# Performance work log

Measured on AMD Instinct MI355X. Metric: run time of the kernel, lower is better.

## Reference

```python
import jax, jax.numpy as jnp
import numpy as np

N_NODES, N_EDGES, D, N_RELS = 50000, 600000, 128, 460


def setup_inputs() -> dict:
    key = jax.random.key(0)
    ks = jax.random.split(key, 8)
    h = jax.random.normal(ks[0], (N_NODES, D), dtype=jnp.float32)
    emb_rel = jax.random.normal(ks[1], (N_RELS, D), dtype=jnp.float32)
    attn_fc_w = jax.random.normal(ks[2], (D, 3 * D), dtype=jnp.float32) * 0.05   # Linear(3D->D), weight [out,in]
    attn_fc2_w = jax.random.normal(ks[3], (1, D), dtype=jnp.float32) * 0.05     # Linear(D->1)
    loop_weight = jax.random.normal(ks[4], (D, D), dtype=jnp.float32) * 0.05
    edge_src = jax.random.randint(ks[5], (N_EDGES,), 0, N_NODES)
    edge_dst = jax.random.randint(ks[6], (N_EDGES,), 0, N_NODES)
    edge_type = jax.random.randint(ks[7], (N_EDGES,), 0, N_RELS)
    return {"h": h, "emb_rel": emb_rel, "attn_fc_w": attn_fc_w,
            "attn_fc2_w": attn_fc2_w, "loop_weight": loop_weight,
            "edge_src": edge_src, "edge_dst": edge_dst, "edge_type": edge_type}


def reference(h, emb_rel, attn_fc_w, attn_fc2_w, loop_weight, edge_src, edge_dst, edge_type):
    n = h.shape[0]
    # --- per-edge gather ---
    hs = h[edge_src]            # [E, D] src features (mailbox 'e_h')
    ht = h[edge_dst]            # [E, D]
    rel = emb_rel[edge_type]    # [E, D]
    # --- concat-MLP attention: leaky_relu(fc2(fc1([hs|ht|rel]))) ---
    z2 = jnp.concatenate([hs, ht, rel], axis=1)          # [E, 3D]
    a = z2 @ attn_fc_w.T                                  # [E, D]
    e = jax.nn.leaky_relu(a @ attn_fc2_w.T)               # [E, 1], slope 0.01 (torch default)
    # --- per-destination segment softmax ---
    m = jax.ops.segment_max(e, edge_dst, num_segments=n)  # [N, 1]
    m = jnp.where(jnp.isfinite(m), m, jnp.float32(0.0))   # empty nodes -> -inf; neutralize
    ex = jnp.exp(e - m[edge_dst])                         # [E, 1]
    den = jax.ops.segment_sum(ex, edge_dst, num_segments=n)
    alpha = ex / den[edge_dst]                            # [E, 1]
    # --- weighted scatter-sum of src features ---
    node_repr = jax.ops.segment_sum(alpha * hs, edge_dst, num_segments=n)  # [N, D]
    # --- self-loop ---
    node_repr = node_repr + h @ loop_weight
    return node_repr
```

## Files before the change

kernel.cpp:

```cpp
#include <hip/hip_runtime.h>

#define N_NODES 50000
#define N_EDGES 600000
#define D 128
#define N_RELS 460
#define CAP_LOG 6

typedef unsigned short u16;
typedef __attribute__((ext_vector_type(8))) short bf16x8;
typedef __attribute__((ext_vector_type(4))) float f32x4;

enum : int {
    OFF_W      = 0,
    OFF_S1     = 384,
    OFF_S2     = 50384,
    OFF_S3     = 100384,
    OFF_COUNTS = 100864,
    OFF_CSR    = 900864,
    OFF_HB     = 4100864,
    OFF_WT     = 7300864,
};

#define NODE_WAVES   12500
#define REL_WAVES    115
#define SCORE_BLOCKS 3154
#define ZERO_BLOCKS  3125
#define FILL_BLOCKS  1172
#define GEMM_BLOCKS  782

__device__ __forceinline__ u16 f2bf(float f) {
    unsigned u = __float_as_uint(f);
    unsigned r = u + 0x7FFFu + ((u >> 16) & 1u);
    return (u16)(r >> 16);
}

__global__ void k_prep(const float* __restrict__ fc1, const float* __restrict__ fc2,
                       const float* __restrict__ W,
                       float* __restrict__ w, u16* __restrict__ wt,
                       int* __restrict__ counts) {
    int b = blockIdx.x, t = threadIdx.x;
    if (b == 0) {
        for (int j = t; j < 3 * D; j += 256) {
            float acc = 0.f;
            for (int k = 0; k < D; ++k) acc += fc2[k] * fc1[k * 3 * D + j];
            w[j] = acc;
        }
    } else if (b <= 64) {
        int i = (b - 1) * 256 + t;
        int k = i >> 7, n = i & 127;
        wt[n * D + k] = f2bf(W[k * D + n]);
    } else {
        int i = (b - 65) * 256 + t;
        if (i < N_NODES * 16) counts[i] = 0;
    }
}

__global__ __launch_bounds__(256) void k_fused(
        const int* __restrict__ src, const int* __restrict__ dst,
        const int* __restrict__ typ, int* __restrict__ counts,
        unsigned* __restrict__ csr,
        const float* __restrict__ h, const float* __restrict__ emb_rel,
        const float* __restrict__ w,
        float* __restrict__ s1, float* __restrict__ s2, float* __restrict__ s3,
        u16* __restrict__ hb, const u16* __restrict__ wt,
        float* __restrict__ out) {
    if (blockIdx.x < FILL_BLOCKS) {
        int i = blockIdx.x * blockDim.x + threadIdx.x;
        if (i >= N_EDGES / 2) return;
        int2 d2  = ((const int2*)dst)[i];
        int2 s2v = ((const int2*)src)[i];
        int2 t2  = ((const int2*)typ)[i];
        int slot0 = atomicAdd(&counts[d2.x << 4], 1);
        int slot1 = atomicAdd(&counts[d2.y << 4], 1);
        csr[(d2.x << CAP_LOG) + slot0] = (unsigned)s2v.x | ((unsigned)t2.x << 16);
        csr[(d2.y << CAP_LOG) + slot1] = (unsigned)s2v.y | ((unsigned)t2.y << 16);
    } else if (blockIdx.x < FILL_BLOCKS + GEMM_BLOCKS) {
        int b = blockIdx.x - FILL_BLOCKS;
        int t = threadIdx.x;
        int wave = t >> 6, lane = t & 63;
        int quad = lane >> 4, m16 = lane & 15;
        int nbase = b * 64 + wave * 16;

        f32x4 acc[8];
        #pragma unroll
        for (int cg = 0; cg < 8; ++cg) acc[cg] = (f32x4){0.f, 0.f, 0.f, 0.f};

        int arow = nbase + m16;
        if (arow >= N_NODES) arow = N_NODES - 1;
        const float* aptr = h + (size_t)arow * D + quad * 8;

        #pragma unroll
        for (int k0 = 0; k0 < D; k0 += 32) {
            float4 a0 = *(const float4*)(aptr + k0);
            float4 a1 = *(const float4*)(aptr + k0 + 4);
            bf16x8 a;
            a[0] = (short)f2bf(a0.x); a[1] = (short)f2bf(a0.y);
            a[2] = (short)f2bf(a0.z); a[3] = (short)f2bf(a0.w);
            a[4] = (short)f2bf(a1.x); a[5] = (short)f2bf(a1.y);
            a[6] = (short)f2bf(a1.z); a[7] = (short)f2bf(a1.w);
            #pragma unroll
            for (int cg = 0; cg < 8; ++cg) {
                bf16x8 bb = *(const bf16x8*)(&wt[(size_t)(cg * 16 + m16) * D + k0 + quad * 8]);
                acc[cg] = __builtin_amdgcn_mfma_f32_16x16x32_bf16(a, bb, acc[cg], 0, 0, 0);
            }
        }
        #pragma unroll
        for (int reg = 0; reg < 4; ++reg) {
            int row = nbase + quad * 4 + reg;
            if (row < N_NODES) {
                #pragma unroll
                for (int cg = 0; cg < 8; ++cg)
                    out[(size_t)row * D + cg * 16 + m16] = acc[cg][reg];
            }
        }
    } else {
        int wv = ((blockIdx.x - FILL_BLOCKS - GEMM_BLOCKS) * blockDim.x + threadIdx.x) >> 6;
        int l  = threadIdx.x & 63;
        int sub = l >> 4;
        int q   = l & 15;
        if (wv < NODE_WAVES) {
            int r = wv * 4 + sub;
            const float* hp = h + (size_t)r * D + q * 8;
            float4 h0 = *(const float4*)hp;
            float4 h1 = *(const float4*)(hp + 4);
            uint4 pk;
            pk.x = (unsigned)f2bf(h0.x) | ((unsigned)f2bf(h0.y) << 16);
            pk.y = (unsigned)f2bf(h0.z) | ((unsigned)f2bf(h0.w) << 16);
            pk.z = (unsigned)f2bf(h1.x) | ((unsigned)f2bf(h1.y) << 16);
            pk.w = (unsigned)f2bf(h1.z) | ((unsigned)f2bf(h1.w) << 16);
            ((uint4*)hb)[(size_t)r * 16 + q] = pk;
            float4 w10 = *(const float4*)(w + q * 8);
            float4 w11 = *(const float4*)(w + q * 8 + 4);
            float4 w20 = *(const float4*)(w + D + q * 8);
            float4 w21 = *(const float4*)(w + D + q * 8 + 4);
            float a1 = h0.x * w10.x + h0.y * w10.y + h0.z * w10.z + h0.w * w10.w
                     + h1.x * w11.x + h1.y * w11.y + h1.z * w11.z + h1.w * w11.w;
            float a2 = h0.x * w20.x + h0.y * w20.y + h0.z * w20.z + h0.w * w20.w
                     + h1.x * w21.x + h1.y * w21.y + h1.z * w21.z + h1.w * w21.w;
            #pragma unroll
            for (int o = 8; o; o >>= 1) { a1 += __shfl_xor(a1, o, 16); a2 += __shfl_xor(a2, o, 16); }
            if (q == 0) { s1[r] = a1; s2[r] = a2; }
        } else if (wv < NODE_WAVES + REL_WAVES) {
            int r = (wv - NODE_WAVES) * 4 + sub;
            const float* rp = emb_rel + (size_t)r * D + q * 8;
            float4 r0 = *(const float4*)rp;
            float4 r1 = *(const float4*)(rp + 4);
            float4 w30 = *(const float4*)(w + 2 * D + q * 8);
            float4 w31 = *(const float4*)(w + 2 * D + q * 8 + 4);
            float a3 = r0.x * w30.x + r0.y * w30.y + r0.z * w30.z + r0.w * w30.w
                     + r1.x * w31.x + r1.y * w31.y + r1.z * w31.z + r1.w * w31.w;
            #pragma unroll
            for (int o = 8; o; o >>= 1) a3 += __shfl_xor(a3, o, 16);
            if (q == 0) s3[r] = a3;
        }
    }
}

__global__ void k_gather(const u16* __restrict__ hb, const int* __restrict__ counts,
                         const unsigned* __restrict__ csr,
                         const float* __restrict__ s1, const float* __restrict__ s2,
                         const float* __restrict__ s3, float* __restrict__ out) {
    int n  = (blockIdx.x * blockDim.x + threadIdx.x) >> 4;
    int gl = threadIdx.x & 15;
    if (n >= N_NODES) return;
    int deg = counts[n << 4];
    if (deg == 0) return;
    int beg = n << CAP_LOG;
    int end = beg + deg;

    float s2n = s2[n];
    float den = 0.f;
    f32x4 accA = {0.f, 0.f, 0.f, 0.f}, accB = {0.f, 0.f, 0.f, 0.f};

    for (int cb = beg; cb < end; cb += 16) {
        int i = cb + gl;
        int msrc = 0; float mex = 0.f;
        if (i < end) {
            unsigned p = csr[i];
            msrc = (int)(p & 0xFFFFu);
            float x = s1[msrc] + s2n + s3[p >> 16];
            float lv = (x > 0.f) ? x : 0.01f * x;
            mex = __expf(lv);
        }
        den += mex;
        int cnt = min(16, end - cb);
        int j = 0;
        for (; j + 3 < cnt; j += 4) {
            int   a0 = __shfl(msrc, j, 16),     a1 = __shfl(msrc, j + 1, 16);
            int   a2 = __shfl(msrc, j + 2, 16), a3 = __shfl(msrc, j + 3, 16);
            float c0 = __shfl(mex, j, 16),      c1 = __shfl(mex, j + 1, 16);
            float c2 = __shfl(mex, j + 2, 16),  c3 = __shfl(mex, j + 3, 16);
            uint4 u0 = ((const uint4*)(hb + (size_t)a0 * D))[gl];
            uint4 u1 = ((const uint4*)(hb + (size_t)a1 * D))[gl];
            uint4 u2 = ((const uint4*)(hb + (size_t)a2 * D))[gl];
            uint4 u3 = ((const uint4*)(hb + (size_t)a3 * D))[gl];
            accA.x += c0 * __uint_as_float(u0.x << 16) + c1 * __uint_as_float(u1.x << 16)
                    + c2 * __uint_as_float(u2.x << 16) + c3 * __uint_as_float(u3.x << 16);
            accA.y += c0 * __uint_as_float(u0.x & 0xFFFF0000u) + c1 * __uint_as_float(u1.x & 0xFFFF0000u)
                    + c2 * __uint_as_float(u2.x & 0xFFFF0000u) + c3 * __uint_as_float(u3.x & 0xFFFF0000u);
            accA.z += c0 * __uint_as_float(u0.y << 16) + c1 * __uint_as_float(u1.y << 16)
                    + c2 * __uint_as_float(u2.y << 16) + c3 * __uint_as_float(u3.y << 16);
            accA.w += c0 * __uint_as_float(u0.y & 0xFFFF0000u) + c1 * __uint_as_float(u1.y & 0xFFFF0000u)
                    + c2 * __uint_as_float(u2.y & 0xFFFF0000u) + c3 * __uint_as_float(u3.y & 0xFFFF0000u);
            accB.x += c0 * __uint_as_float(u0.z << 16) + c1 * __uint_as_float(u1.z << 16)
                    + c2 * __uint_as_float(u2.z << 16) + c3 * __uint_as_float(u3.z << 16);
            accB.y += c0 * __uint_as_float(u0.z & 0xFFFF0000u) + c1 * __uint_as_float(u1.z & 0xFFFF0000u)
                    + c2 * __uint_as_float(u2.z & 0xFFFF0000u) + c3 * __uint_as_float(u3.z & 0xFFFF0000u);
            accB.z += c0 * __uint_as_float(u0.w << 16) + c1 * __uint_as_float(u1.w << 16)
                    + c2 * __uint_as_float(u2.w << 16) + c3 * __uint_as_float(u3.w << 16);
            accB.w += c0 * __uint_as_float(u0.w & 0xFFFF0000u) + c1 * __uint_as_float(u1.w & 0xFFFF0000u)
                    + c2 * __uint_as_float(u2.w & 0xFFFF0000u) + c3 * __uint_as_float(u3.w & 0xFFFF0000u);
        }
        for (; j < cnt; ++j) {
            int   a0 = __shfl(msrc, j, 16);
            float c0 = __shfl(mex, j, 16);
            uint4 u0 = ((const uint4*)(hb + (size_t)a0 * D))[gl];
            accA.x += c0 * __uint_as_float(u0.x << 16);
            accA.y += c0 * __uint_as_float(u0.x & 0xFFFF0000u);
            accA.z += c0 * __uint_as_float(u0.y << 16);
            accA.w += c0 * __uint_as_float(u0.y & 0xFFFF0000u);
            accB.x += c0 * __uint_as_float(u0.z << 16);
            accB.y += c0 * __uint_as_float(u0.z & 0xFFFF0000u);
            accB.z += c0 * __uint_as_float(u0.w << 16);
            accB.w += c0 * __uint_as_float(u0.w & 0xFFFF0000u);
        }
    }
    #pragma unroll
    for (int o = 8; o; o >>= 1) den += __shfl_xor(den, o, 16);
    float inv = 1.f / den;

    float* op = out + (size_t)n * D + gl * 8;
    float4 o0 = *(float4*)op, o1 = *(float4*)(op + 4);
    o0.x += accA.x * inv; o0.y += accA.y * inv; o0.z += accA.z * inv; o0.w += accA.w * inv;
    o1.x += accB.x * inv; o1.y += accB.y * inv; o1.z += accB.z * inv; o1.w += accB.w * inv;
    *(float4*)op = o0; *(float4*)(op + 4) = o1;
}

extern "C" void kernel_launch(void* const* d_in, const int* in_sizes, int n_in,
                              void* d_out, int out_size, void* d_ws, size_t ws_size,
                              hipStream_t stream) {
    const float* h       = (const float*)d_in[0];
    const float* emb_rel = (const float*)d_in[1];
    const float* fc1     = (const float*)d_in[2];
    const float* fc2     = (const float*)d_in[3];
    const float* loopw   = (const float*)d_in[4];
    const int*   esrc    = (const int*)d_in[5];
    const int*   edst    = (const int*)d_in[6];
    const int*   etyp    = (const int*)d_in[7];
    float* out = (float*)d_out;
    float* ws  = (float*)d_ws;

    float*    w       = ws + OFF_W;
    float*    s1      = ws + OFF_S1;
    float*    s2      = ws + OFF_S2;
    float*    s3      = ws + OFF_S3;
    int*      counts  = (int*)(ws + OFF_COUNTS);
    unsigned* csr     = (unsigned*)(ws + OFF_CSR);
    u16*      hb      = (u16*)(ws + OFF_HB);
    u16*      wt      = (u16*)(ws + OFF_WT);

    k_prep<<<1 + 64 + ZERO_BLOCKS, 256, 0, stream>>>(fc1, fc2, loopw, w, wt, counts);

    k_fused<<<FILL_BLOCKS + GEMM_BLOCKS + SCORE_BLOCKS, 256, 0, stream>>>(
        esrc, edst, etyp, counts, csr, h, emb_rel, w, s1, s2, s3, hb, wt, out);

    k_gather<<<(N_NODES * 16 + 255) / 256, 256, 0, stream>>>(
        hb, counts, csr, s1, s2, s3, out);
}
```

Before: 173.8 us.

## Move self-loop GEMM into prep kernel with LDS-staged weights and widen fill/gather

The self-loop GEMM moves from the fused kernel into the prep kernel. Each GEMM block now converts and transposes the loop weight into padded shared memory itself, so the separate global bf16 transposed weight buffer is no longer needed. Count zeroing uses int4 stores across fewer blocks. The CSR fill handles four edges per thread, and the gather loop is unrolled by 8 so more row loads are in flight. The cost is that every GEMM block redoes the 128x128 weight conversion, and the prep kernel becomes heavier while the fused kernel gets lighter.

```diff
diff --git a/kernel.cpp b/kernel.cpp
--- a/kernel.cpp
+++ b/kernel.cpp
@@ -18,15 +18,15 @@
     OFF_COUNTS = 100864,
     OFF_CSR    = 900864,
     OFF_HB     = 4100864,
-    OFF_WT     = 7300864,
 };
 
 #define NODE_WAVES   12500
 #define REL_WAVES    115
 #define SCORE_BLOCKS 3154
-#define ZERO_BLOCKS  3125
-#define FILL_BLOCKS  1172
 #define GEMM_BLOCKS  782
+#define ZERO_BLOCKS  196
+#define FILL_BLOCKS  586
+#define WT_STRIDE    136
 
 __device__ __forceinline__ u16 f2bf(float f) {
     unsigned u = __float_as_uint(f);
@@ -34,52 +34,28 @@
     return (u16)(r >> 16);
 }
 
-__global__ void k_prep(const float* __restrict__ fc1, const float* __restrict__ fc2,
-                       const float* __restrict__ W,
-                       float* __restrict__ w, u16* __restrict__ wt,
-                       int* __restrict__ counts) {
-    int b = blockIdx.x, t = threadIdx.x;
-    if (b == 0) {
-        for (int j = t; j < 3 * D; j += 256) {
-            float acc = 0.f;
-            for (int k = 0; k < D; ++k) acc += fc2[k] * fc1[k * 3 * D + j];
-            w[j] = acc;
-        }
-    } else if (b <= 64) {
-        int i = (b - 1) * 256 + t;
-        int k = i >> 7, n = i & 127;
-        wt[n * D + k] = f2bf(W[k * D + n]);
-    } else {
-        int i = (b - 65) * 256 + t;
-        if (i < N_NODES * 16) counts[i] = 0;
-    }
-}
-
-__global__ __launch_bounds__(256) void k_fused(
-        const int* __restrict__ src, const int* __restrict__ dst,
-        const int* __restrict__ typ, int* __restrict__ counts,
-        unsigned* __restrict__ csr,
-        const float* __restrict__ h, const float* __restrict__ emb_rel,
-        const float* __restrict__ w,
-        float* __restrict__ s1, float* __restrict__ s2, float* __restrict__ s3,
-        u16* __restrict__ hb, const u16* __restrict__ wt,
+__global__ __launch_bounds__(256) void k_prep(
+        const float* __restrict__ fc1, const float* __restrict__ fc2,
+        const float* __restrict__ W, const float* __restrict__ h,
+        float* __restrict__ w, int* __restrict__ counts,
         float* __restrict__ out) {
-    if (blockIdx.x < FILL_BLOCKS) {
-        int i = blockIdx.x * blockDim.x + threadIdx.x;
-        if (i >= N_EDGES / 2) return;
-        int2 d2  = ((const int2*)dst)[i];
-        int2 s2v = ((const int2*)src)[i];
-        int2 t2  = ((const int2*)typ)[i];
-        int slot0 = atomicAdd(&counts[d2.x << 4], 1);
-        int slot1 = atomicAdd(&counts[d2.y << 4], 1);
-        csr[(d2.x << CAP_LOG) + slot0] = (unsigned)s2v.x | ((unsigned)t2.x << 16);
-        csr[(d2.y << CAP_LOG) + slot1] = (unsigned)s2v.y | ((unsigned)t2.y << 16);
-    } else if (blockIdx.x < FILL_BLOCKS + GEMM_BLOCKS) {
-        int b = blockIdx.x - FILL_BLOCKS;
-        int t = threadIdx.x;
+    __shared__ u16 Ws[D * WT_STRIDE];
+    int t = threadIdx.x;
+    if (blockIdx.x < GEMM_BLOCKS) {
+        for (int i = t; i < (D * D) / 4; i += 256) {
+            float4 v = ((const float4*)W)[i];
+            int k  = i >> 5;
+            int n0 = (i & 31) * 4;
+            Ws[(n0 + 0) * WT_STRIDE + k] = f2bf(v.x);
+            Ws[(n0 + 1) * WT_STRIDE + k] = f2bf(v.y);
+            Ws[(n0 + 2) * WT_STRIDE + k] = f2bf(v.z);
+            Ws[(n0 + 3) * WT_STRIDE + k] = f2bf(v.w);
+        }
+        __syncthreads();
+
         int wave = t >> 6, lane = t & 63;
         int quad = lane >> 4, m16 = lane & 15;
-        int nbase = b * 64 + wave * 16;
+        int nbase = blockIdx.x * 64 + wave * 16;
 
         f32x4 acc[8];
         #pragma unroll
@@ -100,7 +76,7 @@
             a[6] = (short)f2bf(a1.z); a[7] = (short)f2bf(a1.w);
             #pragma unroll
             for (int cg = 0; cg < 8; ++cg) {
-                bf16x8 bb = *(const bf16x8*)(&wt[(size_t)(cg * 16 + m16) * D + k0 + quad * 8]);
+                bf16x8 bb = *(const bf16x8*)(&Ws[(cg * 16 + m16) * WT_STRIDE + k0 + quad * 8]);
                 acc[cg] = __builtin_amdgcn_mfma_f32_16x16x32_bf16(a, bb, acc[cg], 0, 0, 0);
             }
         }
@@ -113,8 +89,49 @@
                     out[(size_t)row * D + cg * 16 + m16] = acc[cg][reg];
             }
         }
+    } else if (blockIdx.x < GEMM_BLOCKS + ZERO_BLOCKS) {
+        int base = ((blockIdx.x - GEMM_BLOCKS) * 256 + t) * 4;
+        int i4 = ((blockIdx.x - GEMM_BLOCKS) * 256 + t);
+        #pragma unroll
+        for (int rep = 0; rep < 4; ++rep) {
+            int idx = (i4 * 4 + rep);
+            if (idx * 4 < N_NODES * 16)
+                ((int4*)counts)[idx] = make_int4(0, 0, 0, 0);
+        }
+        (void)base;
     } else {
-        int wv = ((blockIdx.x - FILL_BLOCKS - GEMM_BLOCKS) * blockDim.x + threadIdx.x) >> 6;
+        for (int j = t; j < 3 * D; j += 256) {
+            float acc = 0.f;
+            for (int k = 0; k < D; ++k) acc += fc2[k] * fc1[k * 3 * D + j];
+            w[j] = acc;
+        }
+    }
+}
+
+__global__ __launch_bounds__(256) void k_fused(
+        const int* __restrict__ src, const int* __restrict__ dst,
+        const int* __restrict__ typ, int* __restrict__ counts,
+        unsigned* __restrict__ csr,
+        const float* __restrict__ h, const float* __restrict__ emb_rel,
+        const float* __restrict__ w,
+        float* __restrict__ s1, float* __restrict__ s2, float* __restrict__ s3,
+        u16* __restrict__ hb) {
+    if (blockIdx.x < FILL_BLOCKS) {
+        int i = blockIdx.x * blockDim.x + threadIdx.x;
+        if (i >= N_EDGES / 4) return;
+        int4 d4 = ((const int4*)dst)[i];
+        int4 s4 = ((const int4*)src)[i];
+        int4 t4 = ((const int4*)typ)[i];
+        int sl0 = atomicAdd(&counts[d4.x << 4], 1);
+        int sl1 = atomicAdd(&counts[d4.y << 4], 1);
+        int sl2 = atomicAdd(&counts[d4.z << 4], 1);
+        int sl3 = atomicAdd(&counts[d4.w << 4], 1);
+        csr[(d4.x << CAP_LOG) + sl0] = (unsigned)s4.x | ((unsigned)t4.x << 16);
+        csr[(d4.y << CAP_LOG) + sl1] = (unsigned)s4.y | ((unsigned)t4.y << 16);
+        csr[(d4.z << CAP_LOG) + sl2] = (unsigned)s4.z | ((unsigned)t4.z << 16);
+        csr[(d4.w << CAP_LOG) + sl3] = (unsigned)s4.w | ((unsigned)t4.w << 16);
+    } else {
+        int wv = ((blockIdx.x - FILL_BLOCKS) * blockDim.x + threadIdx.x) >> 6;
         int l  = threadIdx.x & 63;
         int sub = l >> 4;
         int q   = l & 15;
@@ -156,6 +173,16 @@
     }
 }
 
+#define ROWACC(uu, cc)                                                         \
+    accA.x += (cc) * __uint_as_float((uu).x << 16);                            \
+    accA.y += (cc) * __uint_as_float((uu).x & 0xFFFF0000u);                    \
+    accA.z += (cc) * __uint_as_float((uu).y << 16);                            \
+    accA.w += (cc) * __uint_as_float((uu).y & 0xFFFF0000u);                    \
+    accB.x += (cc) * __uint_as_float((uu).z << 16);                            \
+    accB.y += (cc) * __uint_as_float((uu).z & 0xFFFF0000u);                    \
+    accB.z += (cc) * __uint_as_float((uu).w << 16);                            \
+    accB.w += (cc) * __uint_as_float((uu).w & 0xFFFF0000u);
+
 __global__ void k_gather(const u16* __restrict__ hb, const int* __restrict__ counts,
                          const unsigned* __restrict__ csr,
                          const float* __restrict__ s1, const float* __restrict__ s2,
@@ -185,44 +212,37 @@
         den += mex;
         int cnt = min(16, end - cb);
         int j = 0;
+        for (; j + 7 < cnt; j += 8) {
+            int aa[8]; float cc[8]; uint4 uu[8];
+            #pragma unroll
+            for (int u = 0; u < 8; ++u) {
+                aa[u] = __shfl(msrc, j + u, 16);
+                cc[u] = __shfl(mex,  j + u, 16);
+            }
+            #pragma unroll
+            for (int u = 0; u < 8; ++u)
+                uu[u] = ((const uint4*)(hb + (size_t)aa[u] * D))[gl];
+            #pragma unroll
+            for (int u = 0; u < 8; ++u) { ROWACC(uu[u], cc[u]); }
+        }
         for (; j + 3 < cnt; j += 4) {
-            int   a0 = __shfl(msrc, j, 16),     a1 = __shfl(msrc, j + 1, 16);
-            int   a2 = __shfl(msrc, j + 2, 16), a3 = __shfl(msrc, j + 3, 16);
-            float c0 = __shfl(mex, j, 16),      c1 = __shfl(mex, j + 1, 16);
-            float c2 = __shfl(mex, j + 2, 16),  c3 = __shfl(mex, j + 3, 16);
-            uint4 u0 = ((const uint4*)(hb + (size_t)a0 * D))[gl];
-            uint4 u1 = ((const uint4*)(hb + (size_t)a1 * D))[gl];
-            uint4 u2 = ((const uint4*)(hb + (size_t)a2 * D))[gl];
-            uint4 u3 = ((const uint4*)(hb + (size_t)a3 * D))[gl];
-            accA.x += c0 * __uint_as_float(u0.x << 16) + c1 * __uint_as_float(u1.x << 16)
-                    + c2 * __uint_as_float(u2.x << 16) + c3 * __uint_as_float(u3.x << 16);
-            accA.y += c0 * __uint_as_float(u0.x & 0xFFFF0000u) + c1 * __uint_as_float(u1.x & 0xFFFF0000u)
-                    + c2 * __uint_as_float(u2.x & 0xFFFF0000u) + c3 * __uint_as_float(u3.x & 0xFFFF0000u);
-            accA.z += c0 * __uint_as_float(u0.y << 16) + c1 * __uint_as_float(u1.y << 16)
-                    + c2 * __uint_as_float(u2.y << 16) + c3 * __uint_as_float(u3.y << 16);
-            accA.w += c0 * __uint_as_float(u0.y & 0xFFFF0000u) + c1 * __uint_as_float(u1.y & 0xFFFF0000u)
-                    + c2 * __uint_as_float(u2.y & 0xFFFF0000u) + c3 * __uint_as_float(u3.y & 0xFFFF0000u);
-            accB.x += c0 * __uint_as_float(u0.z << 16) + c1 * __uint_as_float(u1.z << 16)
-                    + c2 * __uint_as_float(u2.z << 16) + c3 * __uint_as_float(u3.z << 16);
-            accB.y += c0 * __uint_as_float(u0.z & 0xFFFF0000u) + c1 * __uint_as_float(u1.z & 0xFFFF0000u)
-                    + c2 * __uint_as_float(u2.z & 0xFFFF0000u) + c3 * __uint_as_float(u3.z & 0xFFFF0000u);
-            accB.z += c0 * __uint_as_float(u0.w << 16) + c1 * __uint_as_float(u1.w << 16)
-                    + c2 * __uint_as_float(u2.w << 16) + c3 * __uint_as_float(u3.w << 16);
-            accB.w += c0 * __uint_as_float(u0.w & 0xFFFF0000u) + c1 * __uint_as_float(u1.w & 0xFFFF0000u)
-                    + c2 * __uint_as_float(u2.w & 0xFFFF0000u) + c3 * __uint_as_float(u3.w & 0xFFFF0000u);
+            int aa[4]; float cc[4]; uint4 uu[4];
+            #pragma unroll
+            for (int u = 0; u < 4; ++u) {
+                aa[u] = __shfl(msrc, j + u, 16);
+                cc[u] = __shfl(mex,  j + u, 16);
+            }
+            #pragma unroll
+            for (int u = 0; u < 4; ++u)
+                uu[u] = ((const uint4*)(hb + (size_t)aa[u] * D))[gl];
+            #pragma unroll
+            for (int u = 0; u < 4; ++u) { ROWACC(uu[u], cc[u]); }
         }
         for (; j < cnt; ++j) {
             int   a0 = __shfl(msrc, j, 16);
             float c0 = __shfl(mex, j, 16);
             uint4 u0 = ((const uint4*)(hb + (size_t)a0 * D))[gl];
-            accA.x += c0 * __uint_as_float(u0.x << 16);
-            accA.y += c0 * __uint_as_float(u0.x & 0xFFFF0000u);
-            accA.z += c0 * __uint_as_float(u0.y << 16);
-            accA.w += c0 * __uint_as_float(u0.y & 0xFFFF0000u);
-            accB.x += c0 * __uint_as_float(u0.z << 16);
-            accB.y += c0 * __uint_as_float(u0.z & 0xFFFF0000u);
-            accB.z += c0 * __uint_as_float(u0.w << 16);
-            accB.w += c0 * __uint_as_float(u0.w & 0xFFFF0000u);
+            ROWACC(u0, c0);
         }
     }
     #pragma unroll
@@ -257,12 +277,12 @@
     int*      counts  = (int*)(ws + OFF_COUNTS);
     unsigned* csr     = (unsigned*)(ws + OFF_CSR);
     u16*      hb      = (u16*)(ws + OFF_HB);
-    u16*      wt      = (u16*)(ws + OFF_WT);
-
-    k_prep<<<1 + 64 + ZERO_BLOCKS, 256, 0, stream>>>(fc1, fc2, loopw, w, wt, counts);
-
-    k_fused<<<FILL_BLOCKS + GEMM_BLOCKS + SCORE_BLOCKS, 256, 0, stream>>>(
-        esrc, edst, etyp, counts, csr, h, emb_rel, w, s1, s2, s3, hb, wt, out);
+
+    k_prep<<<GEMM_BLOCKS + ZERO_BLOCKS + 1, 256, 0, stream>>>(
+        fc1, fc2, loopw, h, w, counts, out);
+
+    k_fused<<<FILL_BLOCKS + SCORE_BLOCKS, 256, 0, stream>>>(
+        esrc, edst, etyp, counts, csr, h, emb_rel, w, s1, s2, s3, hb);
 
     k_gather<<<(N_NODES * 16 + 255) / 256, 256, 0, stream>>>(
         hb, counts, csr, s1, s2, s3, out);
```

After: 172.2 us. Within noise of the previous version (-0.9%).
